# Kernel tuning notes

Measured on AMD Instinct MI355X. Metric: run time of the kernel, lower is better.

## Reference

```python
import jax, jax.numpy as jnp
import numpy as np

B, L, D, F, T = 32, 768, 256, 256, 3072
_EPS = 1e-5


def _layernorm(h, g, b):
    mu = jnp.mean(h, axis=-1, keepdims=True)
    var = jnp.var(h, axis=-1, keepdims=True)
    return (h - mu) * jax.lax.rsqrt(var + _EPS) * g + b


def _conv1d(h, w, b):
    # h: [B, L, Cin], w: [K, Cin, Cout] (HIO), padding=1 matches torch Conv1d(padding=1)
    return jax.lax.conv_general_dilated(h, w, (1,), [(1, 1)], dimension_numbers=('NHC', 'HIO', 'NHC')) + b


def setup_inputs() -> dict:
    key = jax.random.key(0)
    ks = jax.random.split(key, 6)
    return {
        'x': jax.random.normal(ks[0], (B, L, D), jnp.float32),
        'target': jax.random.randint(ks[1], (B, L), 0, 4, jnp.int32),
        'mel_max_length': T,
        'conv1_w': jax.random.normal(ks[2], (3, D, F), jnp.float32) * 0.05,
        'conv1_b': jnp.zeros((F,), jnp.float32),
        'ln1_g': jnp.ones((F,), jnp.float32),
        'ln1_b': jnp.zeros((F,), jnp.float32),
        'conv2_w': jax.random.normal(ks[3], (3, F, F), jnp.float32) * 0.05,
        'conv2_b': jnp.zeros((F,), jnp.float32),
        'ln2_g': jnp.ones((F,), jnp.float32),
        'ln2_b': jnp.zeros((F,), jnp.float32),
        'lin_w': jax.random.normal(ks[4], (F, 1), jnp.float32) * 0.05,
        'lin_b': jnp.zeros((1,), jnp.float32),
    }


def reference(x, target, mel_max_length, conv1_w, conv1_b, ln1_g, ln1_b,
              conv2_w, conv2_b, ln2_g, ln2_b, lin_w, lin_b):
    alpha = 1.0
    # DurationPredictor: conv -> relu -> LN -> conv -> relu -> LN -> linear (dropout=0)
    h = _layernorm(jax.nn.relu(_conv1d(x, conv1_w, conv1_b)), ln1_g, ln1_b)
    h = _layernorm(jax.nn.relu(_conv1d(h, conv2_w, conv2_b)), ln2_g, ln2_b)
    dp_out = (h @ lin_w + lin_b)[..., 0]                       # [B, L]
    durations = jnp.exp(dp_out) * alpha                        # [B, L] float
    # Training branch: durations come from target
    dpo = jnp.round(target.astype(jnp.float32) * alpha).astype(jnp.int32)  # [B, L]
    # LR: alignment @ x realized as cumulative-duration searchsorted + gather
    cum = jnp.cumsum(dpo, axis=1)                              # [B, L]
    t = jnp.arange(mel_max_length, dtype=jnp.int32)            # [T]
    idx = jax.vmap(lambda c: jnp.searchsorted(c, t, side='right'))(cum)  # [B, T]
    mask = (t[None, :] < cum[:, -1:]).astype(x.dtype)          # [B, T] zero past total frames
    out = jnp.take_along_axis(x, jnp.clip(idx, 0, x.shape[1] - 1)[:, :, None], axis=1)
    out = out * mask[:, :, None]                               # [B, T, D]
    return (out, dpo, durations)
```

## Files before the change

### kernel.cpp

```cpp
#include <hip/hip_runtime.h>
#include <hip/hip_bf16.h>
#include <math.h>

#define BB 32
#define LL 768
#define DD 256
#define FF 256
#define TT 3072
#define MT 48
#define PAD 262
#define A1R 66

typedef __attribute__((ext_vector_type(8))) short bf16x8;
typedef __attribute__((ext_vector_type(4))) float f32x4;

__device__ inline unsigned short f2b(float f) {
    union { float f; unsigned u; } v; v.f = f;
    unsigned r = (v.u + 0x7FFF + ((v.u >> 16) & 1)) >> 16;
    return (unsigned short)r;
}

#define DPP_ROR_ADD(v, ctrl)                                                   \
    v += __int_as_float(__builtin_amdgcn_update_dpp(                           \
        0, __float_as_int(v), ctrl, 0xF, 0xF, false))

__device__ inline void red16_pair(float& a, float& b) {
    DPP_ROR_ADD(a, 0x128); DPP_ROR_ADD(b, 0x128);
    DPP_ROR_ADD(a, 0x124); DPP_ROR_ADD(b, 0x124);
    DPP_ROR_ADD(a, 0x122); DPP_ROR_ADD(b, 0x122);
    DPP_ROR_ADD(a, 0x121); DPP_ROR_ADD(b, 0x121);
}

__device__ inline float red16_one(float a) {
    DPP_ROR_ADD(a, 0x128);
    DPP_ROR_ADD(a, 0x124);
    DPP_ROR_ADD(a, 0x122);
    DPP_ROR_ADD(a, 0x121);
    return a;
}

__global__ __launch_bounds__(256) void prep_scan_kernel(
    const float* __restrict__ w1, const float* __restrict__ w2,
    unsigned short* __restrict__ wQ1, unsigned short* __restrict__ wQ2,
    const int* __restrict__ target,
    float* __restrict__ out_dpo,
    int* __restrict__ idx_map)
{
    __shared__ int tsum[256];
    const int tid = threadIdx.x;

    if (blockIdx.x < 48) {
        const int layer = blockIdx.x / 24;
        const int s  = blockIdx.x % 24;
        const int kc = s >> 3, c8 = s & 7;
        const float* __restrict__ w = layer ? w2 : w1;
        unsigned short* __restrict__ o = (layer ? wQ2 : wQ1) + s * 8192 + tid * 32;
        const int n = tid;

        alignas(16) unsigned short tmp[32];
#pragma unroll
        for (int q = 0; q < 4; ++q)
#pragma unroll
            for (int j = 0; j < 8; ++j) {
                const int cin = c8 * 32 + q * 8 + j;
                tmp[q * 8 + j] = f2b(w[((size_t)(kc * 256 + cin)) * 256 + n]);
            }
#pragma unroll
        for (int i = 0; i < 4; ++i)
            *reinterpret_cast<uint4*>(o + i * 8) = *reinterpret_cast<const uint4*>(tmp + i * 8);
        return;
    }

    const int b = blockIdx.x - 48;

    const int l = 3 * tid;
    const int v0 = target[b * LL + l];
    const int v1 = target[b * LL + l + 1];
    const int v2 = target[b * LL + l + 2];
    out_dpo[b * LL + l]     = (float)v0;
    out_dpo[b * LL + l + 1] = (float)v1;
    out_dpo[b * LL + l + 2] = (float)v2;

    const int s0 = v0, s1 = v0 + v1, s2 = v0 + v1 + v2;
    tsum[tid] = s2;
    __syncthreads();
    for (int off = 1; off < 256; off <<= 1) {
        int xq = (tid >= off) ? tsum[tid - off] : 0;
        __syncthreads();
        tsum[tid] += xq;
        __syncthreads();
    }
    const int excl = tsum[tid] - s2;

    for (int t = tid; t < TT; t += 256) idx_map[b * TT + t] = -1;
    __syncthreads();

    const int c0 = excl + s0, c1 = excl + s1, c2 = excl + s2;
    for (int t = excl; t < c0 && t < TT; ++t) idx_map[b * TT + t] = l;
    for (int t = c0;   t < c1 && t < TT; ++t) idx_map[b * TT + t] = l + 1;
    for (int t = c1;   t < c2 && t < TT; ++t) idx_map[b * TT + t] = l + 2;
}

__global__ __launch_bounds__(256, 2) void fused_dp_kernel(
    const float* __restrict__ x,
    const unsigned short* __restrict__ wQ1,
    const unsigned short* __restrict__ wQ2,
    const float* __restrict__ c1b, const float* __restrict__ g1, const float* __restrict__ b1,
    const float* __restrict__ c2b, const float* __restrict__ g2, const float* __restrict__ b2,
    const float* __restrict__ lw,  const float* __restrict__ lb,
    float* __restrict__ out_dur)
{
    __shared__ union {
        unsigned short A1[A1R * PAD];
        unsigned short h2[50 * PAD];
    } sm;
    __shared__ float red[4][4][4][4][2];
    __shared__ float redp[4][3][4][4];
    __shared__ float fin[50][2];

    const int tid  = threadIdx.x;
    const int b    = blockIdx.x / (LL / MT);
    const int l0   = (blockIdx.x % (LL / MT)) * MT;
    const int wave = tid >> 6, lane = tid & 63;
    const int quad = lane >> 4, l16 = lane & 15;

    int   cols[4];
    float c1bv[4], g1v[4], b1v[4], c2bv[4], g2v[4], b2v[4], lwv[4];
#pragma unroll
    for (int nt = 0; nt < 4; ++nt) {
        const int c = wave * 64 + nt * 16 + l16;
        cols[nt] = c;
        c1bv[nt] = c1b[c]; g1v[nt] = g1[c]; b1v[nt] = b1[c];
        c2bv[nt] = c2b[c]; g2v[nt] = g2[c]; b2v[nt] = b2[c];
        lwv[nt]  = lw[c];
    }
    const float lbv = lb[0];

    {
        float4 v0[7], v1[7];
        int lr[7];
#pragma unroll
        for (int k = 0; k < 7; ++k) {
            const int q  = tid + (k << 8);
            const int ar = q >> 5;
            const int l  = l0 - 2 + ar;
            lr[k] = (ar < 52 && l >= 0 && l < LL) ? l : -1;
            if (lr[k] >= 0) {
                const float* pp = x + ((size_t)b * LL + lr[k]) * DD + (q & 31) * 8;
                v0[k] = *reinterpret_cast<const float4*>(pp);
                v1[k] = *reinterpret_cast<const float4*>(pp + 4);
            }
        }
#pragma unroll
        for (int k = 0; k < 7; ++k) {
            const int q  = tid + (k << 8);
            const int ar = q >> 5;
            bf16x8 val;
#pragma unroll
            for (int j = 0; j < 8; ++j) val[j] = 0;
            if (lr[k] >= 0) {
                val[0] = (short)f2b(v0[k].x); val[1] = (short)f2b(v0[k].y);
                val[2] = (short)f2b(v0[k].z); val[3] = (short)f2b(v0[k].w);
                val[4] = (short)f2b(v1[k].x); val[5] = (short)f2b(v1[k].y);
                val[6] = (short)f2b(v1[k].z); val[7] = (short)f2b(v1[k].w);
            }
            *reinterpret_cast<bf16x8*>(&sm.A1[ar * PAD + (q & 31) * 8]) = val;
        }
        for (int q = tid; q < 320; q += 256) {
            const int ar = 56 + (q >> 5);
            bf16x8 z;
#pragma unroll
            for (int j = 0; j < 8; ++j) z[j] = 0;
            *reinterpret_cast<bf16x8*>(&sm.A1[ar * PAD + (q & 31) * 8]) = z;
        }
    }
    __syncthreads();

    f32x4 acc1[4][4] = {};
    {
        bf16x8 aE[4], bE[4], aO[4], bO[4];
        auto ld1 = [&](bf16x8* a, bf16x8* bf, int s) {
            const int kc = s >> 3, c8 = s & 7;
#pragma unroll
            for (int mt = 0; mt < 4; ++mt)
                a[mt] = *reinterpret_cast<const bf16x8*>(
                    &sm.A1[(16 * mt + l16 + kc) * PAD + c8 * 32 + quad * 8]);
#pragma unroll
            for (int nt = 0; nt < 4; ++nt)
                bf[nt] = *reinterpret_cast<const bf16x8*>(
                    wQ1 + (size_t)s * 8192 + cols[nt] * 32 + quad * 8);
        };
        auto mm1 = [&](bf16x8* a, bf16x8* bf) {
#pragma unroll
            for (int mt = 0; mt < 4; ++mt)
#pragma unroll
                for (int nt = 0; nt < 4; ++nt)
                    acc1[mt][nt] = __builtin_amdgcn_mfma_f32_16x16x32_bf16(
                        a[mt], bf[nt], acc1[mt][nt], 0, 0, 0);
        };
        ld1(aE, bE, 0);
        for (int s = 0; s < 24; s += 2) {
            ld1(aO, bO, s + 1);
            mm1(aE, bE);
            if (s + 2 < 24) ld1(aE, bE, s + 2);
            mm1(aO, bO);
        }
    }
    __syncthreads();

#pragma unroll
    for (int mt = 0; mt < 4; ++mt)
#pragma unroll
        for (int r = 0; r < 4; ++r) {
            float s1 = 0.f, s2 = 0.f;
#pragma unroll
            for (int nt = 0; nt < 4; ++nt) {
                const float v = fmaxf(acc1[mt][nt][r] + c1bv[nt], 0.f);
                s1 += v; s2 += v * v;
            }
            red16_pair(s1, s2);
            if (l16 == 0) { red[wave][mt][quad][r][0] = s1; red[wave][mt][quad][r][1] = s2; }
        }
    __syncthreads();
    if (tid < 50) {
        const int mt = tid >> 4, q = (tid >> 2) & 3, r = tid & 3;
        const float s1 = red[0][mt][q][r][0] + red[1][mt][q][r][0]
                       + red[2][mt][q][r][0] + red[3][mt][q][r][0];
        const float s2 = red[0][mt][q][r][1] + red[1][mt][q][r][1]
                       + red[2][mt][q][r][1] + red[3][mt][q][r][1];
        const float mu  = s1 * (1.f / 256.f);
        const float var = s2 * (1.f / 256.f) - mu * mu;
        fin[tid][0] = mu;
        fin[tid][1] = rsqrtf(var + 1e-5f);
    }
    __syncthreads();

#pragma unroll
    for (int mt = 0; mt < 4; ++mt)
#pragma unroll
        for (int r = 0; r < 4; ++r) {
            const int rho = 16 * mt + quad * 4 + r;
            if (rho < 50) {
                const int gr = l0 - 1 + rho;
                const float mu = fin[rho][0], rstd = fin[rho][1];
#pragma unroll
                for (int nt = 0; nt < 4; ++nt) {
                    unsigned short hv = 0;
                    if (gr >= 0 && gr < LL) {
                        const float v = fmaxf(acc1[mt][nt][r] + c1bv[nt], 0.f);
                        hv = f2b((v - mu) * rstd * g1v[nt] + b1v[nt]);
                    }
                    sm.h2[rho * PAD + cols[nt]] = hv;
                }
            }
        }
    __syncthreads();

    f32x4 acc2[3][4] = {};
    {
        bf16x8 aE[3], bE[4], aO[3], bO[4];
        auto ld2 = [&](bf16x8* a, bf16x8* bf, int s) {
            const int kc = s >> 3, c8 = s & 7;
#pragma unroll
            for (int mt = 0; mt < 3; ++mt)
                a[mt] = *reinterpret_cast<const bf16x8*>(
                    &sm.h2[(16 * mt + l16 + kc) * PAD + c8 * 32 + quad * 8]);
#pragma unroll
            for (int nt = 0; nt < 4; ++nt)
                bf[nt] = *reinterpret_cast<const bf16x8*>(
                    wQ2 + (size_t)s * 8192 + cols[nt] * 32 + quad * 8);
        };
        auto mm2 = [&](bf16x8* a, bf16x8* bf) {
#pragma unroll
            for (int mt = 0; mt < 3; ++mt)
#pragma unroll
                for (int nt = 0; nt < 4; ++nt)
                    acc2[mt][nt] = __builtin_amdgcn_mfma_f32_16x16x32_bf16(
                        a[mt], bf[nt], acc2[mt][nt], 0, 0, 0);
        };
        ld2(aE, bE, 0);
        for (int s = 0; s < 24; s += 2) {
            ld2(aO, bO, s + 1);
            mm2(aE, bE);
            if (s + 2 < 24) ld2(aE, bE, s + 2);
            mm2(aO, bO);
        }
    }

#pragma unroll
    for (int mt = 0; mt < 3; ++mt)
#pragma unroll
        for (int r = 0; r < 4; ++r) {
            float s1 = 0.f, s2 = 0.f;
#pragma unroll
            for (int nt = 0; nt < 4; ++nt) {
                const float v = fmaxf(acc2[mt][nt][r] + c2bv[nt], 0.f);
                s1 += v; s2 += v * v;
            }
            red16_pair(s1, s2);
            if (l16 == 0) { red[wave][mt][quad][r][0] = s1; red[wave][mt][quad][r][1] = s2; }
        }
    __syncthreads();
    if (tid < MT) {
        const int mt = tid >> 4, q = (tid >> 2) & 3, r = tid & 3;
        const float s1 = red[0][mt][q][r][0] + red[1][mt][q][r][0]
                       + red[2][mt][q][r][0] + red[3][mt][q][r][0];
        const float s2 = red[0][mt][q][r][1] + red[1][mt][q][r][1]
                       + red[2][mt][q][r][1] + red[3][mt][q][r][1];
        const float mu  = s1 * (1.f / 256.f);
        const float var = s2 * (1.f / 256.f) - mu * mu;
        fin[tid][0] = mu;
        fin[tid][1] = rsqrtf(var + 1e-5f);
    }
    __syncthreads();

#pragma unroll
    for (int mt = 0; mt < 3; ++mt)
#pragma unroll
        for (int r = 0; r < 4; ++r) {
            const int rho = 16 * mt + quad * 4 + r;
            const float mu = fin[rho][0], rstd = fin[rho][1];
            float p = 0.f;
#pragma unroll
            for (int nt = 0; nt < 4; ++nt) {
                const float v = fmaxf(acc2[mt][nt][r] + c2bv[nt], 0.f);
                p += ((v - mu) * rstd * g2v[nt] + b2v[nt]) * lwv[nt];
            }
            p = red16_one(p);
            if (l16 == 0) redp[wave][mt][quad][r] = p;
        }
    __syncthreads();
    if (tid < MT) {
        const int mt = tid >> 4, q = (tid >> 2) & 3, r = tid & 3;
        const float dp = redp[0][mt][q][r] + redp[1][mt][q][r]
                       + redp[2][mt][q][r] + redp[3][mt][q][r] + lbv;
        out_dur[(size_t)b * LL + l0 + tid] = expf(dp);
    }
}

__global__ __launch_bounds__(256) void gather_kernel(
    const float* __restrict__ x,
    const int* __restrict__ idx_map,
    float* __restrict__ out)
{
    const int wv = threadIdx.x >> 6, lane = threadIdx.x & 63;
    const int row = blockIdx.x * 4 + wv;
    const int b = row / TT, t = row - b * TT;
    const int idx = idx_map[b * TT + t];
    f32x4 val = {0.f, 0.f, 0.f, 0.f};
    if (idx >= 0)
        val = *reinterpret_cast<const f32x4*>(x + ((size_t)(b * LL + idx)) * DD + lane * 4);
    __builtin_nontemporal_store(val, reinterpret_cast<f32x4*>(out) + (size_t)row * (DD / 4) + lane);
}

extern "C" void kernel_launch(void* const* d_in, const int* in_sizes, int n_in,
                              void* d_out, int out_size, void* d_ws, size_t ws_size,
                              hipStream_t stream)
{
    const float* x      = (const float*)d_in[0];
    const int*   target = (const int*)  d_in[1];
    const float* c1w = (const float*)d_in[3];
    const float* c1b = (const float*)d_in[4];
    const float* g1  = (const float*)d_in[5];
    const float* b1  = (const float*)d_in[6];
    const float* c2w = (const float*)d_in[7];
    const float* c2b = (const float*)d_in[8];
    const float* g2  = (const float*)d_in[9];
    const float* b2  = (const float*)d_in[10];
    const float* lw  = (const float*)d_in[11];
    const float* lb  = (const float*)d_in[12];

    float* out0    = (float*)d_out;
    float* out_dpo = out0 + (size_t)BB * TT * DD;
    float* out_dur = out_dpo + (size_t)BB * LL;

    char* ws = (char*)d_ws;
    unsigned short* wQ1 = (unsigned short*)ws;                 ws += (size_t)24 * 8192 * 2;
    unsigned short* wQ2 = (unsigned short*)ws;                 ws += (size_t)24 * 8192 * 2;
    int* idx_map        = (int*)ws;

    prep_scan_kernel<<<48 + BB, 256, 0, stream>>>(
        c1w, c2w, wQ1, wQ2, target, out_dpo, idx_map);

    fused_dp_kernel<<<BB * (LL / MT), 256, 0, stream>>>(
        x, wQ1, wQ2, c1b, g1, b1, c2b, g2, b2, lw, lb, out_dur);

    gather_kernel<<<BB * TT / 4, 256, 0, stream>>>(x, idx_map, out0);
}
```

Before: 195.3 us.

## Split conv GEMMs by rows per wave so LayerNorm reductions stay in-wave

Each wave now owns a 16-row M tile and all 256 output columns, where before it owned a 64-column slice of every row. LayerNorm statistics and the final linear dot product can then be reduced inside a wave, which removes the cross-wave shared-memory reduction arrays and several block barriers. The cost is that every wave must load the full weight slice per K step, so B-operand global traffic is four times higher. The larger accumulator and B-register arrays raise register pressure, and one wave idles during the second conv.

After: 229.4 us. +17.4%, slower.

```diff
diff --git a/kernel.cpp b/kernel.cpp
--- a/kernel.cpp
+++ b/kernel.cpp
@@ -114,27 +114,12 @@
         unsigned short A1[A1R * PAD];
         unsigned short h2[50 * PAD];
     } sm;
-    __shared__ float red[4][4][4][4][2];
-    __shared__ float redp[4][3][4][4];
-    __shared__ float fin[50][2];
 
     const int tid  = threadIdx.x;
     const int b    = blockIdx.x / (LL / MT);
     const int l0   = (blockIdx.x % (LL / MT)) * MT;
     const int wave = tid >> 6, lane = tid & 63;
     const int quad = lane >> 4, l16 = lane & 15;
-
-    int   cols[4];
-    float c1bv[4], g1v[4], b1v[4], c2bv[4], g2v[4], b2v[4], lwv[4];
-#pragma unroll
-    for (int nt = 0; nt < 4; ++nt) {
-        const int c = wave * 64 + nt * 16 + l16;
-        cols[nt] = c;
-        c1bv[nt] = c1b[c]; g1v[nt] = g1[c]; b1v[nt] = b1[c];
-        c2bv[nt] = c2b[c]; g2v[nt] = g2[c]; b2v[nt] = b2[c];
-        lwv[nt]  = lw[c];
-    }
-    const float lbv = lb[0];
 
     {
         float4 v0[7], v1[7];
@@ -176,27 +161,23 @@
     }
     __syncthreads();
 
-    f32x4 acc1[4][4] = {};
+    f32x4 acc1[16] = {};
     {
-        bf16x8 aE[4], bE[4], aO[4], bO[4];
-        auto ld1 = [&](bf16x8* a, bf16x8* bf, int s) {
+        bf16x8 aE, aO, bE[16], bO[16];
+        auto ld1 = [&](bf16x8& a, bf16x8* bf, int s) {
             const int kc = s >> 3, c8 = s & 7;
-#pragma unroll
-            for (int mt = 0; mt < 4; ++mt)
-                a[mt] = *reinterpret_cast<const bf16x8*>(
-                    &sm.A1[(16 * mt + l16 + kc) * PAD + c8 * 32 + quad * 8]);
-#pragma unroll
-            for (int nt = 0; nt < 4; ++nt)
+            a = *reinterpret_cast<const bf16x8*>(
+                &sm.A1[(16 * wave + l16 + kc) * PAD + c8 * 32 + quad * 8]);
+#pragma unroll
+            for (int nt = 0; nt < 16; ++nt)
                 bf[nt] = *reinterpret_cast<const bf16x8*>(
-                    wQ1 + (size_t)s * 8192 + cols[nt] * 32 + quad * 8);
+                    wQ1 + (size_t)s * 8192 + (nt * 16 + l16) * 32 + quad * 8);
         };
-        auto mm1 = [&](bf16x8* a, bf16x8* bf) {
-#pragma unroll
-            for (int mt = 0; mt < 4; ++mt)
-#pragma unroll
-                for (int nt = 0; nt < 4; ++nt)
-                    acc1[mt][nt] = __builtin_amdgcn_mfma_f32_16x16x32_bf16(
-                        a[mt], bf[nt], acc1[mt][nt], 0, 0, 0);
+        auto mm1 = [&](bf16x8& a, bf16x8* bf) {
+#pragma unroll
+            for (int nt = 0; nt < 16; ++nt)
+                acc1[nt] = __builtin_amdgcn_mfma_f32_16x16x32_bf16(
+                    a, bf[nt], acc1[nt], 0, 0, 0);
         };
         ld1(aE, bE, 0);
         for (int s = 0; s < 24; s += 2) {
@@ -206,77 +187,70 @@
             mm1(aO, bO);
         }
     }
-    __syncthreads();
-
-#pragma unroll
-    for (int mt = 0; mt < 4; ++mt)
-#pragma unroll
-        for (int r = 0; r < 4; ++r) {
-            float s1 = 0.f, s2 = 0.f;
-#pragma unroll
-            for (int nt = 0; nt < 4; ++nt) {
-                const float v = fmaxf(acc1[mt][nt][r] + c1bv[nt], 0.f);
-                s1 += v; s2 += v * v;
-            }
-            red16_pair(s1, s2);
-            if (l16 == 0) { red[wave][mt][quad][r][0] = s1; red[wave][mt][quad][r][1] = s2; }
-        }
-    __syncthreads();
-    if (tid < 50) {
-        const int mt = tid >> 4, q = (tid >> 2) & 3, r = tid & 3;
-        const float s1 = red[0][mt][q][r][0] + red[1][mt][q][r][0]
-                       + red[2][mt][q][r][0] + red[3][mt][q][r][0];
-        const float s2 = red[0][mt][q][r][1] + red[1][mt][q][r][1]
-                       + red[2][mt][q][r][1] + red[3][mt][q][r][1];
+
+    float c1bv[16], g1v[16], b1v[16];
+#pragma unroll
+    for (int nt = 0; nt < 16; ++nt) {
+        const int c = nt * 16 + l16;
+        c1bv[nt] = c1b[c]; g1v[nt] = g1[c]; b1v[nt] = b1[c];
+    }
+    float mu1[4], rs1[4];
+#pragma unroll
+    for (int r = 0; r < 4; ++r) {
+        float s1 = 0.f, s2 = 0.f;
+#pragma unroll
+        for (int nt = 0; nt < 16; ++nt) {
+            const float v = fmaxf(acc1[nt][r] + c1bv[nt], 0.f);
+            s1 += v; s2 += v * v;
+        }
+        red16_pair(s1, s2);
         const float mu  = s1 * (1.f / 256.f);
         const float var = s2 * (1.f / 256.f) - mu * mu;
-        fin[tid][0] = mu;
-        fin[tid][1] = rsqrtf(var + 1e-5f);
-    }
-    __syncthreads();
-
-#pragma unroll
-    for (int mt = 0; mt < 4; ++mt)
-#pragma unroll
-        for (int r = 0; r < 4; ++r) {
-            const int rho = 16 * mt + quad * 4 + r;
-            if (rho < 50) {
-                const int gr = l0 - 1 + rho;
-                const float mu = fin[rho][0], rstd = fin[rho][1];
-#pragma unroll
-                for (int nt = 0; nt < 4; ++nt) {
-                    unsigned short hv = 0;
-                    if (gr >= 0 && gr < LL) {
-                        const float v = fmaxf(acc1[mt][nt][r] + c1bv[nt], 0.f);
-                        hv = f2b((v - mu) * rstd * g1v[nt] + b1v[nt]);
-                    }
-                    sm.h2[rho * PAD + cols[nt]] = hv;
+        mu1[r] = mu;
+        rs1[r] = rsqrtf(var + 1e-5f);
+    }
+    __syncthreads();
+
+#pragma unroll
+    for (int r = 0; r < 4; ++r) {
+        const int rho = 16 * wave + quad * 4 + r;
+        if (rho < 50) {
+            const int gr = l0 - 1 + rho;
+            if (gr >= 0 && gr < LL) {
+#pragma unroll
+                for (int nt = 0; nt < 16; ++nt) {
+                    const float v = fmaxf(acc1[nt][r] + c1bv[nt], 0.f);
+                    sm.h2[rho * PAD + nt * 16 + l16] =
+                        f2b((v - mu1[r]) * rs1[r] * g1v[nt] + b1v[nt]);
                 }
-            }
-        }
-    __syncthreads();
-
-    f32x4 acc2[3][4] = {};
+            } else {
+#pragma unroll
+                for (int nt = 0; nt < 16; ++nt)
+                    sm.h2[rho * PAD + nt * 16 + l16] = 0;
+            }
+        }
+    }
+    __syncthreads();
+
+    if (wave >= 3) return;
+
+    f32x4 acc2[16] = {};
     {
-        bf16x8 aE[3], bE[4], aO[3], bO[4];
-        auto ld2 = [&](bf16x8* a, bf16x8* bf, int s) {
+        bf16x8 aE, aO, bE[16], bO[16];
+        auto ld2 = [&](bf16x8& a, bf16x8* bf, int s) {
             const int kc = s >> 3, c8 = s & 7;
-#pragma unroll
-            for (int mt = 0; mt < 3; ++mt)
-                a[mt] = *reinterpret_cast<const bf16x8*>(
-                    &sm.h2[(16 * mt + l16 + kc) * PAD + c8 * 32 + quad * 8]);
-#pragma unroll
-            for (int nt = 0; nt < 4; ++nt)
+            a = *reinterpret_cast<const bf16x8*>(
+                &sm.h2[(16 * wave + l16 + kc) * PAD + c8 * 32 + quad * 8]);
+#pragma unroll
+            for (int nt = 0; nt < 16; ++nt)
                 bf[nt] = *reinterpret_cast<const bf16x8*>(
-                    wQ2 + (size_t)s * 8192 + cols[nt] * 32 + quad * 8);
+                    wQ2 + (size_t)s * 8192 + (nt * 16 + l16) * 32 + quad * 8);
         };
-        auto mm2 = [&](bf16x8* a, bf16x8* bf) {
-#pragma unroll
-            for (int mt = 0; mt < 3; ++mt)
-#pragma unroll
-                for (int nt = 0; nt < 4; ++nt)
-                    acc2[mt][nt] = __builtin_amdgcn_mfma_f32_16x16x32_bf16(
-                        a[mt], bf[nt], acc2[mt][nt], 0, 0, 0);
+        auto mm2 = [&](bf16x8& a, bf16x8* bf) {
+#pragma unroll
+            for (int nt = 0; nt < 16; ++nt)
+                acc2[nt] = __builtin_amdgcn_mfma_f32_16x16x32_bf16(
+                    a, bf[nt], acc2[nt], 0, 0, 0);
         };
         ld2(aE, bE, 0);
         for (int s = 0; s < 24; s += 2) {
@@ -287,54 +261,38 @@
         }
     }
 
-#pragma unroll
-    for (int mt = 0; mt < 3; ++mt)
+    {
+        float c2bv[16], g2v[16], b2v[16], lwv[16];
+#pragma unroll
+        for (int nt = 0; nt < 16; ++nt) {
+            const int c = nt * 16 + l16;
+            c2bv[nt] = c2b[c]; g2v[nt] = g2[c]; b2v[nt] = b2[c]; lwv[nt] = lw[c];
+        }
+        const float lbv = lb[0];
 #pragma unroll
         for (int r = 0; r < 4; ++r) {
             float s1 = 0.f, s2 = 0.f;
 #pragma unroll
-            for (int nt = 0; nt < 4; ++nt) {
-                const float v = fmaxf(acc2[mt][nt][r] + c2bv[nt], 0.f);
+            for (int nt = 0; nt < 16; ++nt) {
+                const float v = fmaxf(acc2[nt][r] + c2bv[nt], 0.f);
                 s1 += v; s2 += v * v;
             }
             red16_pair(s1, s2);
-            if (l16 == 0) { red[wave][mt][quad][r][0] = s1; red[wave][mt][quad][r][1] = s2; }
-        }
-    __syncthreads();
-    if (tid < MT) {
-        const int mt = tid >> 4, q = (tid >> 2) & 3, r = tid & 3;
-        const float s1 = red[0][mt][q][r][0] + red[1][mt][q][r][0]
-                       + red[2][mt][q][r][0] + red[3][mt][q][r][0];
-        const float s2 = red[0][mt][q][r][1] + red[1][mt][q][r][1]
-                       + red[2][mt][q][r][1] + red[3][mt][q][r][1];
-        const float mu  = s1 * (1.f / 256.f);
-        const float var = s2 * (1.f / 256.f) - mu * mu;
-        fin[tid][0] = mu;
-        fin[tid][1] = rsqrtf(var + 1e-5f);
-    }
-    __syncthreads();
-
-#pragma unroll
-    for (int mt = 0; mt < 3; ++mt)
-#pragma unroll
-        for (int r = 0; r < 4; ++r) {
-            const int rho = 16 * mt + quad * 4 + r;
-            const float mu = fin[rho][0], rstd = fin[rho][1];
+            const float mu  = s1 * (1.f / 256.f);
+            const float var = s2 * (1.f / 256.f) - mu * mu;
+            const float rstd = rsqrtf(var + 1e-5f);
             float p = 0.f;
 #pragma unroll
-            for (int nt = 0; nt < 4; ++nt) {
-                const float v = fmaxf(acc2[mt][nt][r] + c2bv[nt], 0.f);
+            for (int nt = 0; nt < 16; ++nt) {
+                const float v = fmaxf(acc2[nt][r] + c2bv[nt], 0.f);
                 p += ((v - mu) * rstd * g2v[nt] + b2v[nt]) * lwv[nt];
             }
             p = red16_one(p);
-            if (l16 == 0) redp[wave][mt][quad][r] = p;
-        }
-    __syncthreads();
-    if (tid < MT) {
-        const int mt = tid >> 4, q = (tid >> 2) & 3, r = tid & 3;
-        const float dp = redp[0][mt][q][r] + redp[1][mt][q][r]
-                       + redp[2][mt][q][r] + redp[3][mt][q][r] + lbv;
-        out_dur[(size_t)b * LL + l0 + tid] = expf(dp);
+            if (l16 == 0) {
+                const int rho = 16 * wave + quad * 4 + r;
+                out_dur[(size_t)b * LL + l0 + rho] = expf(p + lbv);
+            }
+        }
     }
 }
 
```
